# Kernel optimization log

Measured on AMD Instinct MI355X. Metric: run time of the kernel, lower is better.

Reference implementation:

```python
import jax, jax.numpy as jnp
import numpy as np

FACTOR = 2
DIM = 3
F3 = FACTOR ** DIM            # 8
B = 2                          # batch size
S = 128                        # cubic spatial shape (spatial_shape = [S, S, S])
N = 262144                     # number of active voxels
C = 32                         # feature channels
MAXS = (S + FACTOR - 1) // FACTOR  # 64, downsampled grid extent per dim
# OFFSET per torch code: cumprod of MAX reversed, reversed, + [1]
OFFSET = (MAXS ** 3, MAXS ** 2, MAXS, 1)


def setup_inputs() -> dict:
    rng = np.random.default_rng(0)
    # unique voxel coords: sample N distinct cells from the B x S^3 grid
    lin = rng.permutation(B * S ** 3)[:N].astype(np.int64)
    b = lin // (S ** 3)
    r = lin % (S ** 3)
    x = r // (S * S)
    y = (r // S) % S
    z = r % S
    coords = jnp.asarray(np.stack([b, x, y, z], axis=-1), dtype=jnp.int32)  # [N, 4]
    feats = jax.random.normal(jax.random.key(0), (N, C), dtype=jnp.float32)
    return {"feats": feats, "coords": coords}


def reference(feats, coords):
    c = coords.astype(jnp.int32)
    down = c[:, 1:] // FACTOR          # [N, 3] downsampled spatial coords
    sub = c[:, 1:] % FACTOR            # [N, 3] position within factor^3 cell
    # subidx = sum(sub[..., i] * factor**i), i=0 -> x
    subidx = sub[:, 0] + sub[:, 1] * FACTOR + sub[:, 2] * (FACTOR ** 2)
    # linear code over (batch, dx, dy, dz)
    code = (c[:, 0] * OFFSET[0] + down[:, 0] * OFFSET[1]
            + down[:, 1] * OFFSET[2] + down[:, 2] * OFFSET[3])
    # unique with static size=N (M_unique <= N); pad with out-of-range sentinel
    code_u, idx = jnp.unique(code, return_inverse=True, size=N,
                             fill_value=B * MAXS ** 3)
    idx = idx.reshape(-1)
    new_coords = jnp.stack(
        [code_u // OFFSET[0]]
        + [(code_u // OFFSET[i + 1]) % MAXS for i in range(DIM)], axis=-1)
    # scatter feats into channel-expanded buffer; padded rows stay zero
    buf = jnp.zeros((N * F3, C), dtype=feats.dtype).at[idx * F3 + subidx].set(feats)
    new_feats = buf.reshape(N, F3 * C)   # [N_pad, factor^3 * C]
    return new_feats, new_coords
```

## Files before the change

kernel.cpp:

```cpp
#include <hip/hip_runtime.h>

typedef unsigned int u32;
typedef float __attribute__((ext_vector_type(4))) f4;
typedef unsigned int __attribute__((ext_vector_type(4))) u4;

static constexpr u32 NCODES = 524288u;
static constexpr u32 ZB = 1024;

__device__ __forceinline__ u32 code_of(int4 c) {
  return ((u32)c.x << 18) + ((u32)(c.y >> 1) << 12) +
         ((u32)(c.z >> 1) << 6) + (u32)(c.w >> 1);
}

__device__ __forceinline__ void zero_chunk(f4* __restrict__ base, u32 zb, u32 t,
                                           u32 nIter) {
  const f4 z = {0.f, 0.f, 0.f, 0.f};
  u32 i0 = zb * 256u + t;
  for (u32 k = 0; k < nIter; ++k)
    __builtin_nontemporal_store(z, base + i0 + k * (ZB * 256u));
}

__global__ void k_A(f4* __restrict__ out, u32 n, u4* __restrict__ marks,
                    f4* __restrict__ zbase, u32 zIter) {
  u32 b = blockIdx.x, t = threadIdx.x;
  u32 sentB = n / 1024u;
  if (b < NCODES / 4u / 256u) {
    const u4 z = {0u, 0u, 0u, 0u};
    __builtin_nontemporal_store(z, marks + b * 256u + t);
  } else if (b < NCODES / 4u / 256u + sentB) {
    f4* outc = out + (size_t)n * 64u;
    u32 i = (b - NCODES / 4u / 256u) * 256u + t;
    const f4 s4 = {2.f, 0.f, 0.f, 0.f};
    u32 span = sentB * 256u;
    for (u32 k = 0; k < 4u; ++k)
      __builtin_nontemporal_store(s4, outc + i + k * span);
  } else {
    zero_chunk(zbase, b - (NCODES / 4u / 256u + sentB), t, zIter);
  }
}

__global__ void k_B(const int4* __restrict__ coords, u32* __restrict__ mark, u32 n,
                    f4* __restrict__ zbase, u32 zIter) {
  u32 b = blockIdx.x, t = threadIdx.x;
  u32 mb = n / 256u;
  if (b < mb) {
    u32 i = b * 256u + t;
    mark[code_of(coords[i])] = 1u;
  } else {
    zero_chunk(zbase, b - mb, t, zIter);
  }
}

__global__ void k_C(const u32* __restrict__ mark, u32* __restrict__ bsum,
                    f4* __restrict__ zbase, u32 zIter) {
  u32 b = blockIdx.x, t = threadIdx.x;
  if (b >= 512u) { zero_chunk(zbase, b - 512u, t, zIter); return; }
  uint4 m = ((const uint4*)mark)[b * 256u + t];
  u32 s = m.x + m.y + m.z + m.w;
  for (int d = 32; d > 0; d >>= 1) s += __shfl_down(s, d, 64);
  __shared__ u32 ws4[4];
  if ((t & 63u) == 0u) ws4[t >> 6] = s;
  __syncthreads();
  if (t == 0) bsum[b] = ws4[0] + ws4[1] + ws4[2] + ws4[3];
}

__device__ __forceinline__ void wrc(float* __restrict__ outc, u32 r, u32 code) {
  float4 p;
  p.x = (float)(code >> 18);
  p.y = (float)((code >> 12) & 63u);
  p.z = (float)((code >> 6) & 63u);
  p.w = (float)(code & 63u);
  ((float4*)outc)[r] = p;
}

__global__ void k_D(u32* __restrict__ codes, const u32* __restrict__ bsum,
                    float* __restrict__ outc, f4* __restrict__ zbase, u32 zIter) {
  u32 b = blockIdx.x, t = threadIdx.x;
  if (b >= 512u) { zero_chunk(zbase, b - 512u, t, zIter); return; }

  u32 v0 = bsum[t], v1 = bsum[t + 256u];
  u32 s = (t < b ? v0 : 0u) + (t + 256u < b ? v1 : 0u);
  for (int d = 32; d > 0; d >>= 1) s += __shfl_down(s, d, 64);
  __shared__ u32 ws4[4];
  if ((t & 63u) == 0u) ws4[t >> 6] = s;
  __syncthreads();
  u32 boff = ws4[0] + ws4[1] + ws4[2] + ws4[3];

  uint4 m = ((const uint4*)codes)[b * 256u + t];
  u32 tsum = m.x + m.y + m.z + m.w;
  u32 incl = tsum;
  u32 lane = t & 63u;
  for (int d = 1; d < 64; d <<= 1) {
    u32 v = __shfl_up(incl, d, 64);
    if (lane >= (u32)d) incl += v;
  }
  __shared__ u32 wsum[4];
  if (lane == 63u) wsum[t >> 6] = incl;
  __syncthreads();
  u32 woff = boff;
  for (u32 w = 0; w < (t >> 6); ++w) woff += wsum[w];
  u32 e0 = woff + incl - tsum;
  u32 e1 = e0 + m.x, e2 = e1 + m.y, e3 = e2 + m.z;
  ((uint4*)codes)[b * 256u + t] = make_uint4(e0, e1, e2, e3);
  u32 base = b * 1024u + t * 4u;
  if (m.x) wrc(outc, e0, base + 0u);
  if (m.y) wrc(outc, e1, base + 1u);
  if (m.z) wrc(outc, e2, base + 2u);
  if (m.w) wrc(outc, e3, base + 3u);
}

__global__ void k_E(const float4* __restrict__ feats, const int4* __restrict__ coords,
                    const u32* __restrict__ rank, float* __restrict__ out, int n8) {
  int tid = blockIdx.x * blockDim.x + threadIdx.x;
  if (tid >= n8) return;
  int row = tid >> 3, q = tid & 7;
  int4 c = coords[row];
  u32 code = code_of(c);
  u32 sub = (u32)(c.y & 1) + ((u32)(c.z & 1) << 1) + ((u32)(c.w & 1) << 2);
  float4 f = feats[tid];
  ((float4*)out)[((size_t)rank[code] * 8u + sub) * 8u + (u32)q] = f;
}

extern "C" void kernel_launch(void* const* d_in, const int* in_sizes, int n_in,
                              void* d_out, int out_size, void* d_ws, size_t ws_size,
                              hipStream_t stream) {
  const float* feats = (const float*)d_in[0];
  const int* coords  = (const int*)d_in[1];
  u32 n = (u32)(in_sizes[1] / 4);
  f4* out4 = (f4*)d_out;
  float* outc = (float*)d_out + (size_t)n * 256u;

  u32* codes = (u32*)d_ws;
  u32* bsum  = codes + NCODES;

  u32 feats4 = n * 64u;
  u32 chunk  = feats4 / 4u;
  u32 zIter  = chunk / (ZB * 256u);
  u32 markZB = NCODES / 4u / 256u;
  u32 sentB  = n / 1024u;

  k_A<<<markZB + sentB + ZB, 256, 0, stream>>>(out4, n, (u4*)codes,
                                               out4 + 0u * chunk, zIter);
  k_B<<<n / 256u + ZB, 256, 0, stream>>>((const int4*)coords, codes, n,
                                         out4 + 1u * chunk, zIter);
  k_C<<<512u + ZB, 256, 0, stream>>>(codes, bsum, out4 + 2u * chunk, zIter);
  k_D<<<512u + ZB, 256, 0, stream>>>(codes, bsum, outc, out4 + 3u * chunk, zIter);
  k_E<<<(n * 8u + 255u) / 256u, 256, 0, stream>>>((const float4*)feats,
                                                  (const int4*)coords, codes,
                                                  (float*)d_out, (int)(n * 8u));
}
```

Before: 318.4 us.

## Drop mark-clearing pass using a tag sentinel and merge into three-stage pipeline

The mark array is no longer zeroed each call. Active codes are written as 0xFFFFFFFF, and the count and scan stages test for that tag instead of summing 0/1 flags. This removes a full kernel launch and the clearing traffic, and the output zeroing is redistributed over the remaining three stages. The scatter kernel also uses nontemporal loads and stores. The risk is that correctness now depends on the workspace never holding the tag value from earlier contents, which holds for leftover ranks but not for arbitrary initial memory.

```diff
diff --git a/kernel.cpp b/kernel.cpp
--- a/kernel.cpp
+++ b/kernel.cpp
@@ -5,58 +5,43 @@
 typedef unsigned int __attribute__((ext_vector_type(4))) u4;
 
 static constexpr u32 NCODES = 524288u;
-static constexpr u32 ZB = 1024;
+static constexpr u32 ZB = 1024u;
+static constexpr u32 TAG = 0xFFFFFFFFu;
 
 __device__ __forceinline__ u32 code_of(int4 c) {
   return ((u32)c.x << 18) + ((u32)(c.y >> 1) << 12) +
          ((u32)(c.z >> 1) << 6) + (u32)(c.w >> 1);
 }
 
-__device__ __forceinline__ void zero_chunk(f4* __restrict__ base, u32 zb, u32 t,
-                                           u32 nIter) {
+__device__ __forceinline__ void zero_n(f4* __restrict__ base, u32 zb, u32 t, u32 cnt) {
   const f4 z = {0.f, 0.f, 0.f, 0.f};
-  u32 i0 = zb * 256u + t;
-  for (u32 k = 0; k < nIter; ++k)
-    __builtin_nontemporal_store(z, base + i0 + k * (ZB * 256u));
+  for (u32 i = zb * 256u + t; i < cnt; i += ZB * 256u)
+    __builtin_nontemporal_store(z, base + i);
 }
 
-__global__ void k_A(f4* __restrict__ out, u32 n, u4* __restrict__ marks,
-                    f4* __restrict__ zbase, u32 zIter) {
+__global__ void k_1(const int4* __restrict__ coords, u32* __restrict__ mark, u32 n,
+                    f4* __restrict__ outc4, f4* __restrict__ zbase, u32 zcnt) {
   u32 b = blockIdx.x, t = threadIdx.x;
-  u32 sentB = n / 1024u;
-  if (b < NCODES / 4u / 256u) {
-    const u4 z = {0u, 0u, 0u, 0u};
-    __builtin_nontemporal_store(z, marks + b * 256u + t);
-  } else if (b < NCODES / 4u / 256u + sentB) {
-    f4* outc = out + (size_t)n * 64u;
-    u32 i = (b - NCODES / 4u / 256u) * 256u + t;
+  u32 mb = n / 256u, sb = n / 1024u;
+  if (b < mb) {
+    mark[code_of(coords[b * 256u + t])] = TAG;
+  } else if (b < mb + sb) {
+    u32 i = (b - mb) * 256u + t;
     const f4 s4 = {2.f, 0.f, 0.f, 0.f};
-    u32 span = sentB * 256u;
+    u32 span = sb * 256u;
     for (u32 k = 0; k < 4u; ++k)
-      __builtin_nontemporal_store(s4, outc + i + k * span);
+      __builtin_nontemporal_store(s4, outc4 + i + k * span);
   } else {
-    zero_chunk(zbase, b - (NCODES / 4u / 256u + sentB), t, zIter);
+    zero_n(zbase, b - mb - sb, t, zcnt);
   }
 }
 
-__global__ void k_B(const int4* __restrict__ coords, u32* __restrict__ mark, u32 n,
-                    f4* __restrict__ zbase, u32 zIter) {
+__global__ void k_2(const u4* __restrict__ mark, u32* __restrict__ bsum,
+                    f4* __restrict__ zbase, u32 zcnt) {
   u32 b = blockIdx.x, t = threadIdx.x;
-  u32 mb = n / 256u;
-  if (b < mb) {
-    u32 i = b * 256u + t;
-    mark[code_of(coords[i])] = 1u;
-  } else {
-    zero_chunk(zbase, b - mb, t, zIter);
-  }
-}
-
-__global__ void k_C(const u32* __restrict__ mark, u32* __restrict__ bsum,
-                    f4* __restrict__ zbase, u32 zIter) {
-  u32 b = blockIdx.x, t = threadIdx.x;
-  if (b >= 512u) { zero_chunk(zbase, b - 512u, t, zIter); return; }
-  uint4 m = ((const uint4*)mark)[b * 256u + t];
-  u32 s = m.x + m.y + m.z + m.w;
+  if (b >= 512u) { zero_n(zbase, b - 512u, t, zcnt); return; }
+  u4 m = mark[b * 256u + t];
+  u32 s = (m.x == TAG) + (m.y == TAG) + (m.z == TAG) + (m.w == TAG);
   for (int d = 32; d > 0; d >>= 1) s += __shfl_down(s, d, 64);
   __shared__ u32 ws4[4];
   if ((t & 63u) == 0u) ws4[t >> 6] = s;
@@ -65,18 +50,15 @@
 }
 
 __device__ __forceinline__ void wrc(float* __restrict__ outc, u32 r, u32 code) {
-  float4 p;
-  p.x = (float)(code >> 18);
-  p.y = (float)((code >> 12) & 63u);
-  p.z = (float)((code >> 6) & 63u);
-  p.w = (float)(code & 63u);
-  ((float4*)outc)[r] = p;
+  f4 p = {(float)(code >> 18), (float)((code >> 12) & 63u),
+          (float)((code >> 6) & 63u), (float)(code & 63u)};
+  __builtin_nontemporal_store(p, (f4*)outc + r);
 }
 
-__global__ void k_D(u32* __restrict__ codes, const u32* __restrict__ bsum,
-                    float* __restrict__ outc, f4* __restrict__ zbase, u32 zIter) {
+__global__ void k_3(u32* __restrict__ codes, const u32* __restrict__ bsum,
+                    float* __restrict__ outc, f4* __restrict__ zbase, u32 zcnt) {
   u32 b = blockIdx.x, t = threadIdx.x;
-  if (b >= 512u) { zero_chunk(zbase, b - 512u, t, zIter); return; }
+  if (b >= 512u) { zero_n(zbase, b - 512u, t, zcnt); return; }
 
   u32 v0 = bsum[t], v1 = bsum[t + 256u];
   u32 s = (t < b ? v0 : 0u) + (t + 256u < b ? v1 : 0u);
@@ -86,8 +68,9 @@
   __syncthreads();
   u32 boff = ws4[0] + ws4[1] + ws4[2] + ws4[3];
 
-  uint4 m = ((const uint4*)codes)[b * 256u + t];
-  u32 tsum = m.x + m.y + m.z + m.w;
+  u4 m = ((const u4*)codes)[b * 256u + t];
+  u32 p0 = (m.x == TAG), p1 = (m.y == TAG), p2 = (m.z == TAG), p3 = (m.w == TAG);
+  u32 tsum = p0 + p1 + p2 + p3;
   u32 incl = tsum;
   u32 lane = t & 63u;
   for (int d = 1; d < 64; d <<= 1) {
@@ -100,25 +83,26 @@
   u32 woff = boff;
   for (u32 w = 0; w < (t >> 6); ++w) woff += wsum[w];
   u32 e0 = woff + incl - tsum;
-  u32 e1 = e0 + m.x, e2 = e1 + m.y, e3 = e2 + m.z;
-  ((uint4*)codes)[b * 256u + t] = make_uint4(e0, e1, e2, e3);
+  u32 e1 = e0 + p0, e2 = e1 + p1, e3 = e2 + p2;
+  u4 r = {e0, e1, e2, e3};
+  ((u4*)codes)[b * 256u + t] = r;
   u32 base = b * 1024u + t * 4u;
-  if (m.x) wrc(outc, e0, base + 0u);
-  if (m.y) wrc(outc, e1, base + 1u);
-  if (m.z) wrc(outc, e2, base + 2u);
-  if (m.w) wrc(outc, e3, base + 3u);
+  if (p0) wrc(outc, e0, base + 0u);
+  if (p1) wrc(outc, e1, base + 1u);
+  if (p2) wrc(outc, e2, base + 2u);
+  if (p3) wrc(outc, e3, base + 3u);
 }
 
-__global__ void k_E(const float4* __restrict__ feats, const int4* __restrict__ coords,
-                    const u32* __restrict__ rank, float* __restrict__ out, int n8) {
-  int tid = blockIdx.x * blockDim.x + threadIdx.x;
+__global__ void k_4(const f4* __restrict__ feats, const int4* __restrict__ coords,
+                    const u32* __restrict__ rank, f4* __restrict__ out, u32 n8) {
+  u32 tid = blockIdx.x * 256u + threadIdx.x;
   if (tid >= n8) return;
-  int row = tid >> 3, q = tid & 7;
+  u32 row = tid >> 3, q = tid & 7u;
   int4 c = coords[row];
   u32 code = code_of(c);
   u32 sub = (u32)(c.y & 1) + ((u32)(c.z & 1) << 1) + ((u32)(c.w & 1) << 2);
-  float4 f = feats[tid];
-  ((float4*)out)[((size_t)rank[code] * 8u + sub) * 8u + (u32)q] = f;
+  f4 f = __builtin_nontemporal_load(feats + tid);
+  __builtin_nontemporal_store(f, out + ((size_t)rank[code] * 8u + sub) * 8u + q);
 }
 
 extern "C" void kernel_launch(void* const* d_in, const int* in_sizes, int n_in,
@@ -134,18 +118,15 @@
   u32* bsum  = codes + NCODES;
 
   u32 feats4 = n * 64u;
-  u32 chunk  = feats4 / 4u;
-  u32 zIter  = chunk / (ZB * 256u);
-  u32 markZB = NCODES / 4u / 256u;
-  u32 sentB  = n / 1024u;
+  u32 c1 = feats4 / 3u;
+  u32 c2 = c1;
+  u32 c3 = feats4 - 2u * c1;
+  u32 mb = n / 256u, sb = n / 1024u;
 
-  k_A<<<markZB + sentB + ZB, 256, 0, stream>>>(out4, n, (u4*)codes,
-                                               out4 + 0u * chunk, zIter);
-  k_B<<<n / 256u + ZB, 256, 0, stream>>>((const int4*)coords, codes, n,
-                                         out4 + 1u * chunk, zIter);
-  k_C<<<512u + ZB, 256, 0, stream>>>(codes, bsum, out4 + 2u * chunk, zIter);
-  k_D<<<512u + ZB, 256, 0, stream>>>(codes, bsum, outc, out4 + 3u * chunk, zIter);
-  k_E<<<(n * 8u + 255u) / 256u, 256, 0, stream>>>((const float4*)feats,
-                                                  (const int4*)coords, codes,
-                                                  (float*)d_out, (int)(n * 8u));
+  k_1<<<mb + sb + ZB, 256, 0, stream>>>((const int4*)coords, codes, n,
+                                        (f4*)outc, out4, c1);
+  k_2<<<512u + ZB, 256, 0, stream>>>((const u4*)codes, bsum, out4 + c1, c2);
+  k_3<<<512u + ZB, 256, 0, stream>>>(codes, bsum, outc, out4 + c1 + c2, c3);
+  k_4<<<(n * 8u) / 256u, 256, 0, stream>>>((const f4*)feats, (const int4*)coords,
+                                           codes, out4, n * 8u);
 }
```

Result: no change. 318.0 us (-0.1%).
